# Optimization experiments

Hardware: AMD Instinct MI355X
Metric: run time of the kernel (lower is better)

Reference implementation:

```python
import jax, jax.numpy as jnp
import numpy as np
import math

D_MODEL, D_K, D_V, H = 512, 64, 64, 8

def setup_inputs() -> dict:
    key = jax.random.key(0)
    ks = jax.random.split(key, 8)
    B, L = 2, 4096
    q = jax.random.normal(ks[0], (B, L, D_MODEL), dtype=jnp.float32)
    k = jax.random.normal(ks[1], (B, L, D_MODEL), dtype=jnp.float32)
    v = jax.random.normal(ks[2], (B, L, D_MODEL), dtype=jnp.float32)
    attention_mask = jnp.ones((B, L), dtype=jnp.int32)
    s = 1.0 / math.sqrt(D_MODEL)
    Wq = jax.random.uniform(ks[3], (D_MODEL, H * D_K), dtype=jnp.float32, minval=-s, maxval=s)
    Wk = jax.random.uniform(ks[4], (D_MODEL, H * D_K), dtype=jnp.float32, minval=-s, maxval=s)
    Wv = jax.random.uniform(ks[5], (D_MODEL, H * D_V), dtype=jnp.float32, minval=-s, maxval=s)
    so = 1.0 / math.sqrt(H * D_V)
    Wo = jax.random.uniform(ks[6], (H * D_V, D_MODEL), dtype=jnp.float32, minval=-so, maxval=so)
    return {"q": q, "k": k, "v": v, "attention_mask": attention_mask,
            "Wq": Wq, "Wk": Wk, "Wv": Wv, "Wo": Wo}

def reference(q, k, v, attention_mask, Wq, Wk, Wv, Wo):
    B, L, _ = q.shape
    scale = 1.0 / math.sqrt(D_K)
    # project and split heads: [B, H, L, d]
    qh = (q @ Wq).reshape(B, L, H, D_K).transpose(0, 2, 1, 3)
    kh = (k @ Wk).reshape(B, L, H, D_K).transpose(0, 2, 1, 3)
    vh = (v @ Wv).reshape(B, L, H, D_V).transpose(0, 2, 1, 3)
    score = jnp.einsum('bhqd,bhkd->bhqk', qh, kh) * scale  # [B,H,L,L]
    mask = attention_mask[:, None, None, :]  # [B,1,1,L]
    score = jnp.where(mask == 0, -jnp.inf, score)
    attn = jax.nn.softmax(score, axis=-1)
    out = jnp.einsum('bhqk,bhkd->bhqd', attn, vh)
    out = out.transpose(0, 2, 1, 3).reshape(B, L, H * D_V)
    return out @ Wo
```

## Files before the change

### kernel.cpp

```cpp
#include <hip/hip_runtime.h>

typedef short bf16x8 __attribute__((ext_vector_type(8)));
typedef float f32x4 __attribute__((ext_vector_type(4)));
typedef unsigned short u16x8 __attribute__((ext_vector_type(8)));

static __device__ __forceinline__ unsigned short f2bf(float f) {
  unsigned int x = __builtin_bit_cast(unsigned int, f);
  x += 0x7FFFu + ((x >> 16) & 1u);
  return (unsigned short)(x >> 16);
}
static __device__ __forceinline__ unsigned int pk2bf(float a, float b) {
  unsigned int ia = __builtin_bit_cast(unsigned int, a) + 0x8000u;
  unsigned int ib = __builtin_bit_cast(unsigned int, b) + 0x8000u;
  return __builtin_amdgcn_perm(ib, ia, 0x07060302u);
}
static __device__ __forceinline__ void gl2lds16(const unsigned short* g, unsigned short* l) {
  __builtin_amdgcn_global_load_lds(
      (const __attribute__((address_space(1))) unsigned int*)g,
      (__attribute__((address_space(3))) unsigned int*)l, 16, 0, 0);
}

__global__ __launch_bounds__(256) void cvt3(const float* __restrict__ q, const float* __restrict__ k,
                                            const float* __restrict__ v,
                                            unsigned short* __restrict__ qo, unsigned short* __restrict__ ko,
                                            unsigned short* __restrict__ vo) {
  const float* src = (blockIdx.y == 0) ? q : (blockIdx.y == 1) ? k : v;
  unsigned short* dst = (blockIdx.y == 0) ? qo : (blockIdx.y == 1) ? ko : vo;
  int i = (blockIdx.x * 256 + threadIdx.x) * 8;
  float4 a = *(const float4*)(src + i);
  float4 b = *(const float4*)(src + i + 4);
  uint4 pk;
  pk.x = pk2bf(a.x, a.y); pk.y = pk2bf(a.z, a.w);
  pk.z = pk2bf(b.x, b.y); pk.w = pk2bf(b.z, b.w);
  *(uint4*)(dst + i) = pk;
}

__global__ __launch_bounds__(256) void wtrans4(const float* __restrict__ Wq, const float* __restrict__ Wk,
                                               const float* __restrict__ Wv, const float* __restrict__ Wo,
                                               unsigned short* __restrict__ WT) {
  __shared__ __align__(16) float T[64 * 68];
  const int z = blockIdx.z;
  const float* W = (z == 0) ? Wq : (z == 1) ? Wk : (z == 2) ? Wv : Wo;
  unsigned short* out = WT + (size_t)z * 512 * 512;
  const int k0 = blockIdx.x * 64, n0 = blockIdx.y * 64;
  const int tid = threadIdx.x;
#pragma unroll
  for (int i = 0; i < 4; ++i) {
    int chunk = i * 256 + tid;
    int row = chunk >> 4, fc = chunk & 15;
    *(float4*)(T + row * 68 + fc * 4) =
        *(const float4*)(W + (size_t)(k0 + row) * 512 + n0 + fc * 4);
  }
  __syncthreads();
#pragma unroll
  for (int i = 0; i < 2; ++i) {
    int chunk = i * 256 + tid;
    int nr = chunk >> 3, kc = chunk & 7;
    u16x8 v;
#pragma unroll
    for (int j = 0; j < 8; ++j) v[j] = f2bf(T[(kc * 8 + j) * 68 + nr]);
    *(u16x8*)(out + (size_t)(n0 + nr) * 512 + k0 + kc * 8) = v;
  }
}

__global__ __launch_bounds__(256) void gemm_qkv(const unsigned short* __restrict__ Aq,
                                                const unsigned short* __restrict__ Ak,
                                                const unsigned short* __restrict__ Av,
                                                const unsigned short* __restrict__ Bt,
                                                unsigned short* __restrict__ C,
                                                float qscale) {
  __shared__ __align__(16) unsigned short Abuf[2][128 * 64];
  __shared__ __align__(16) unsigned short Bbuf[2][64 * 64];
  const int K = 512, LDC = 1536;
  const unsigned short* A = (blockIdx.y < 8) ? Aq : (blockIdx.y < 16) ? Ak : Av;
  const float scale = (blockIdx.y < 8) ? qscale : 1.0f;
  const int tid = threadIdx.x;
  const int wid = tid >> 6, lane = tid & 63, quad = lane >> 4, li = lane & 15;
  const int bm = blockIdx.x * 128, bn = blockIdx.y * 64;
  const int wm = wid * 32;
  const unsigned short* ga[4]; int oa[4];
  const unsigned short* gb[2]; int ob[2];
#pragma unroll
  for (int i = 0; i < 4; ++i) {
    int lam = i * 256 + wid * 64 + lane;
    int r = lam >> 3, c = (lam & 7) ^ (r & 7);
    ga[i] = A + (size_t)(bm + r) * K + c * 8;
    oa[i] = lam * 8;
  }
#pragma unroll
  for (int i = 0; i < 2; ++i) {
    int lam = i * 256 + wid * 64 + lane;
    int r = lam >> 3, c = (lam & 7) ^ (r & 7);
    gb[i] = Bt + (size_t)(bn + r) * K + c * 8;
    ob[i] = lam * 8;
  }
#pragma unroll
  for (int i = 0; i < 4; ++i) { gl2lds16(ga[i], &Abuf[0][oa[i]]); ga[i] += 64; }
#pragma unroll
  for (int i = 0; i < 2; ++i) { gl2lds16(gb[i], &Bbuf[0][ob[i]]); gb[i] += 64; }

  f32x4 acc[2][4] = {};
  const int sw = li & 7;
  for (int s = 0; s < 8; ++s) {
    __builtin_amdgcn_s_barrier();
    if (s + 1 < 8) {
      int p = (s + 1) & 1;
#pragma unroll
      for (int i = 0; i < 4; ++i) { gl2lds16(ga[i], &Abuf[p][oa[i]]); ga[i] += 64; }
#pragma unroll
      for (int i = 0; i < 2; ++i) { gl2lds16(gb[i], &Bbuf[p][ob[i]]); gb[i] += 64; }
      asm volatile("s_waitcnt vmcnt(6)" ::: "memory");
    } else {
      asm volatile("s_waitcnt vmcnt(0)" ::: "memory");
    }
    __builtin_amdgcn_s_barrier();
    __builtin_amdgcn_sched_barrier(0);
    const unsigned short* As = &Abuf[s & 1][0];
    const unsigned short* Bs = &Bbuf[s & 1][0];
#pragma unroll
    for (int kk = 0; kk < 2; ++kk) {
      bf16x8 af[2], bfr[4];
#pragma unroll
      for (int t = 0; t < 2; ++t)
        af[t] = *(const bf16x8*)(As + (wm + t * 16 + li) * 64 + (((kk * 4 + quad) ^ sw) * 8));
#pragma unroll
      for (int t = 0; t < 4; ++t)
        bfr[t] = *(const bf16x8*)(Bs + (t * 16 + li) * 64 + (((kk * 4 + quad) ^ sw) * 8));
#pragma unroll
      for (int mt = 0; mt < 2; ++mt)
#pragma unroll
        for (int nt = 0; nt < 4; ++nt)
          acc[mt][nt] = __builtin_amdgcn_mfma_f32_16x16x32_bf16(af[mt], bfr[nt], acc[mt][nt], 0, 0, 0);
    }
  }
#pragma unroll
  for (int mt = 0; mt < 2; ++mt)
#pragma unroll
    for (int nt = 0; nt < 4; ++nt) {
      int r0 = bm + wm + mt * 16 + quad * 4;
      int c  = bn + nt * 16 + li;
#pragma unroll
      for (int r = 0; r < 4; ++r)
        C[(size_t)(r0 + r) * LDC + c] = f2bf(acc[mt][nt][r] * scale);
    }
}

__global__ __launch_bounds__(256) void gemm_o(const unsigned short* __restrict__ A,
                                              const unsigned short* __restrict__ Bt,
                                              float* __restrict__ Cf) {
  __shared__ __align__(16) unsigned short Abuf[2][128 * 64];
  __shared__ __align__(16) unsigned short Bbuf[2][64 * 64];
  const int K = 512, LDC = 512;
  const int tid = threadIdx.x;
  const int wid = tid >> 6, lane = tid & 63, quad = lane >> 4, li = lane & 15;
  const int bm = blockIdx.x * 128, bn = blockIdx.y * 64;
  const int wm = wid * 32;
  const unsigned short* ga[4]; int oa[4];
  const unsigned short* gb[2]; int ob[2];
#pragma unroll
  for (int i = 0; i < 4; ++i) {
    int lam = i * 256 + wid * 64 + lane;
    int r = lam >> 3, c = (lam & 7) ^ (r & 7);
    ga[i] = A + (size_t)(bm + r) * K + c * 8;
    oa[i] = lam * 8;
  }
#pragma unroll
  for (int i = 0; i < 2; ++i) {
    int lam = i * 256 + wid * 64 + lane;
    int r = lam >> 3, c = (lam & 7) ^ (r & 7);
    gb[i] = Bt + (size_t)(bn + r) * K + c * 8;
    ob[i] = lam * 8;
  }
#pragma unroll
  for (int i = 0; i < 4; ++i) { gl2lds16(ga[i], &Abuf[0][oa[i]]); ga[i] += 64; }
#pragma unroll
  for (int i = 0; i < 2; ++i) { gl2lds16(gb[i], &Bbuf[0][ob[i]]); gb[i] += 64; }

  f32x4 acc[2][4] = {};
  const int sw = li & 7;
  for (int s = 0; s < 8; ++s) {
    __builtin_amdgcn_s_barrier();
    if (s + 1 < 8) {
      int p = (s + 1) & 1;
#pragma unroll
      for (int i = 0; i < 4; ++i) { gl2lds16(ga[i], &Abuf[p][oa[i]]); ga[i] += 64; }
#pragma unroll
      for (int i = 0; i < 2; ++i) { gl2lds16(gb[i], &Bbuf[p][ob[i]]); gb[i] += 64; }
      asm volatile("s_waitcnt vmcnt(6)" ::: "memory");
    } else {
      asm volatile("s_waitcnt vmcnt(0)" ::: "memory");
    }
    __builtin_amdgcn_s_barrier();
    __builtin_amdgcn_sched_barrier(0);
    const unsigned short* As = &Abuf[s & 1][0];
    const unsigned short* Bs = &Bbuf[s & 1][0];
#pragma unroll
    for (int kk = 0; kk < 2; ++kk) {
      bf16x8 af[2], bfr[4];
#pragma unroll
      for (int t = 0; t < 2; ++t)
        af[t] = *(const bf16x8*)(As + (wm + t * 16 + li) * 64 + (((kk * 4 + quad) ^ sw) * 8));
#pragma unroll
      for (int t = 0; t < 4; ++t)
        bfr[t] = *(const bf16x8*)(Bs + (t * 16 + li) * 64 + (((kk * 4 + quad) ^ sw) * 8));
#pragma unroll
      for (int mt = 0; mt < 2; ++mt)
#pragma unroll
        for (int nt = 0; nt < 4; ++nt)
          acc[mt][nt] = __builtin_amdgcn_mfma_f32_16x16x32_bf16(af[mt], bfr[nt], acc[mt][nt], 0, 0, 0);
    }
  }
#pragma unroll
  for (int mt = 0; mt < 2; ++mt)
#pragma unroll
    for (int nt = 0; nt < 4; ++nt) {
      int r0 = bm + wm + mt * 16 + quad * 4;
      int c  = bn + nt * 16 + li;
#pragma unroll
      for (int r = 0; r < 4; ++r)
        Cf[(size_t)(r0 + r) * LDC + c] = acc[mt][nt][r];
    }
}

__global__ __launch_bounds__(256) void vtrans(const unsigned short* __restrict__ qkv,
                                              unsigned short* __restrict__ vt) {
  __shared__ __align__(16) unsigned short T[64 * 72];
  const int kt = blockIdx.x;
  const int bh = blockIdx.y;
  const int b = bh >> 3, h = bh & 7;
  const int tid = threadIdx.x;
#pragma unroll
  for (int i = 0; i < 2; ++i) {
    int chunk = i * 256 + tid;
    int row = chunk >> 3, c8 = chunk & 7;
    *(uint4*)(T + row * 72 + c8 * 8) =
        *(const uint4*)(qkv + (size_t)(b * 4096 + kt * 64 + row) * 1536 + 1024 + h * 64 + c8 * 8);
  }
  __syncthreads();
#pragma unroll
  for (int i = 0; i < 2; ++i) {
    int chunk = i * 256 + tid;
    int dr = chunk >> 3, c8 = chunk & 7;
    u16x8 v;
#pragma unroll
    for (int j = 0; j < 8; ++j) v[j] = T[(c8 * 8 + j) * 72 + dr];
    *(u16x8*)(vt + (size_t)(bh * 64 + dr) * 4096 + kt * 64 + c8 * 8) = v;
  }
}

__global__ __launch_bounds__(512) void attn(const unsigned short* __restrict__ qkv,
                                            const unsigned short* __restrict__ vt,
                                            const int* __restrict__ mask,
                                            unsigned short* __restrict__ obuf) {
  __shared__ __align__(16) unsigned short Kbuf[2][64 * 64];
  __shared__ __align__(16) unsigned short Vbuf[2][64 * 64];
  __shared__ __align__(16) unsigned short Psh[8][16 * 72];
  __shared__ __align__(16) unsigned short MskBits[256];
  const int qt = blockIdx.x, h = blockIdx.y, b = blockIdx.z;
  const int tid = threadIdx.x;
  const int wid = tid >> 6, lane = tid & 63, quad = lane >> 4, li = lane & 15;
  const size_t tok0 = (size_t)b * 4096;

  if (tid < 256) {
    const int4* mp = (const int4*)(mask + b * 4096 + tid * 16);
    unsigned int bits = 0;
#pragma unroll
    for (int j = 0; j < 4; ++j) {
      int4 m4 = mp[j];
      bits |= (m4.x ? 1u : 0u) << (j * 4 + 0);
      bits |= (m4.y ? 1u : 0u) << (j * 4 + 1);
      bits |= (m4.z ? 1u : 0u) << (j * 4 + 2);
      bits |= (m4.w ? 1u : 0u) << (j * 4 + 3);
    }
    MskBits[tid] = (unsigned short)bits;
  }

  const unsigned short* qp = qkv + (tok0 + qt * 128 + wid * 16 + li) * 1536 + h * 64;
  bf16x8 bq0 = *(const bf16x8*)(qp + quad * 8);
  bf16x8 bq1 = *(const bf16x8*)(qp + 32 + quad * 8);

  const unsigned short* kbase = qkv + tok0 * 1536 + 512 + h * 64;
  const unsigned short* vbase = vt + (size_t)(b * 8 + h) * 64 * 4096;
  const int wk = wid & 3;
  const int lam0 = wk * 128 + lane, lam1 = lam0 + 64;
  const int r0 = lam0 >> 3, c0 = (lam0 & 7) ^ (r0 & 7);
  const int r1 = lam1 >> 3, c1 = (lam1 & 7) ^ (r1 & 7);
  const unsigned short *g0, *g1;
  size_t kstride;
  unsigned short *lb0, *lb1;
  if (wid < 4) {
    g0 = kbase + (size_t)r0 * 1536 + c0 * 8;
    g1 = kbase + (size_t)r1 * 1536 + c1 * 8;
    kstride = (size_t)64 * 1536;
    lb0 = &Kbuf[0][0]; lb1 = &Kbuf[1][0];
  } else {
    g0 = vbase + (size_t)r0 * 4096 + c0 * 8;
    g1 = vbase + (size_t)r1 * 4096 + c1 * 8;
    kstride = 64;
    lb0 = &Vbuf[0][0]; lb1 = &Vbuf[1][0];
  }
  const int o0 = lam0 * 8, o1 = lam1 * 8;

  gl2lds16(g0, lb0 + o0);
  gl2lds16(g1, lb0 + o1);
  g0 += kstride; g1 += kstride;

  f32x4 lacc = {};
  f32x4 accO[4] = {};
  unsigned short* Pw = &Psh[wid][0];
  const int sw = li & 7;

  asm volatile("s_waitcnt lgkmcnt(0)" ::: "memory");

  for (int t = 0; t < 64; ++t) {
    __builtin_amdgcn_s_barrier();
    if (t < 63) {
      unsigned short* lb = ((t + 1) & 1) ? lb1 : lb0;
      gl2lds16(g0, lb + o0);
      gl2lds16(g1, lb + o1);
      g0 += kstride; g1 += kstride;
      asm volatile("s_waitcnt vmcnt(2)" ::: "memory");
    } else {
      asm volatile("s_waitcnt vmcnt(0)" ::: "memory");
    }
    __builtin_amdgcn_s_barrier();
    __builtin_amdgcn_sched_barrier(0);
    const unsigned short* Ks = &Kbuf[t & 1][0];
    const unsigned short* Vs = &Vbuf[t & 1][0];

    f32x4 s[4];
    __builtin_amdgcn_s_setprio(1);
#pragma unroll
    for (int kb = 0; kb < 4; ++kb) {
      const unsigned short* kr = Ks + (kb * 16 + li) * 64;
      bf16x8 ak0 = *(const bf16x8*)(kr + ((quad ^ sw) * 8));
      bf16x8 ak1 = *(const bf16x8*)(kr + (((4 + quad) ^ sw) * 8));
      f32x4 z = {};
      z = __builtin_amdgcn_mfma_f32_16x16x32_bf16(ak0, bq0, z, 0, 0, 0);
      z = __builtin_amdgcn_mfma_f32_16x16x32_bf16(ak1, bq1, z, 0, 0, 0);
      s[kb] = z;
    }
    __builtin_amdgcn_s_setprio(0);
    unsigned long long mbits = *(const unsigned long long*)(MskBits + t * 4);
    if (mbits != ~0ull) {
#pragma unroll
      for (int kb = 0; kb < 4; ++kb)
#pragma unroll
        for (int r = 0; r < 4; ++r) {
          int key = kb * 16 + quad * 4 + r;
          if (!((mbits >> key) & 1ull)) s[kb][r] = -1e30f;
        }
    }
#pragma unroll
    for (int kb = 0; kb < 4; ++kb) {
#pragma unroll
      for (int r = 0; r < 4; ++r) s[kb][r] = __builtin_amdgcn_exp2f(s[kb][r]);
      lacc += s[kb];
      uint2 pk;
      pk.x = pk2bf(s[kb][0], s[kb][1]);
      pk.y = pk2bf(s[kb][2], s[kb][3]);
      *(uint2*)(Pw + li * 72 + kb * 16 + quad * 4) = pk;
    }
    bf16x8 p0 = *(const bf16x8*)(Pw + li * 72 + quad * 8);
    bf16x8 p1 = *(const bf16x8*)(Pw + li * 72 + 32 + quad * 8);
    __builtin_amdgcn_s_setprio(1);
#pragma unroll
    for (int dc = 0; dc < 4; ++dc) {
      const unsigned short* vr = Vs + (dc * 16 + li) * 64;
      bf16x8 bv0 = *(const bf16x8*)(vr + ((quad ^ sw) * 8));
      bf16x8 bv1 = *(const bf16x8*)(vr + (((4 + quad) ^ sw) * 8));
      accO[dc] = __builtin_amdgcn_mfma_f32_16x16x32_bf16(p0, bv0, accO[dc], 0, 0, 0);
      accO[dc] = __builtin_amdgcn_mfma_f32_16x16x32_bf16(p1, bv1, accO[dc], 0, 0, 0);
    }
    __builtin_amdgcn_s_setprio(0);
  }
  float lt = lacc[0] + lacc[1] + lacc[2] + lacc[3];
  lt += __shfl_xor(lt, 16);
  lt += __shfl_xor(lt, 32);
  float lv0 = 1.f / __shfl(lt, quad * 4 + 0);
  float lv1 = 1.f / __shfl(lt, quad * 4 + 1);
  float lv2 = 1.f / __shfl(lt, quad * 4 + 2);
  float lv3 = 1.f / __shfl(lt, quad * 4 + 3);
#pragma unroll
  for (int dc = 0; dc < 4; ++dc) {
    size_t r0q = tok0 + qt * 128 + wid * 16 + quad * 4;
    size_t col = h * 64 + dc * 16 + li;
    obuf[(r0q + 0) * 512 + col] = f2bf(accO[dc][0] * lv0);
    obuf[(r0q + 1) * 512 + col] = f2bf(accO[dc][1] * lv1);
    obuf[(r0q + 2) * 512 + col] = f2bf(accO[dc][2] * lv2);
    obuf[(r0q + 3) * 512 + col] = f2bf(accO[dc][3] * lv3);
  }
}

extern "C" void kernel_launch(void* const* d_in, const int* in_sizes, int n_in,
                              void* d_out, int out_size, void* d_ws, size_t ws_size,
                              hipStream_t stream) {
  const float* q  = (const float*)d_in[0];
  const float* k  = (const float*)d_in[1];
  const float* v  = (const float*)d_in[2];
  const int* mask = (const int*)d_in[3];
  const float* Wq = (const float*)d_in[4];
  const float* Wk = (const float*)d_in[5];
  const float* Wv = (const float*)d_in[6];
  const float* Wo = (const float*)d_in[7];
  float* out = (float*)d_out;

  char* ws = (char*)d_ws;
  const size_t SA = (size_t)8192 * 512 * 2;
  unsigned short* qbf  = (unsigned short*)(ws);
  unsigned short* kbf  = (unsigned short*)(ws + SA);
  unsigned short* vbf  = (unsigned short*)(ws + 2 * SA);
  unsigned short* qkvh = (unsigned short*)(ws + 3 * SA);
  unsigned short* wAll = (unsigned short*)(ws + 6 * SA);
  unsigned short* woT  = wAll + (size_t)3 * 512 * 512;
  unsigned short* vtb  = qbf;
  unsigned short* ob   = kbf;

  dim3 cg(2048, 3);
  cvt3<<<cg, 256, 0, stream>>>(q, k, v, qbf, kbf, vbf);
  dim3 wg(8, 8, 4);
  wtrans4<<<wg, 256, 0, stream>>>(Wq, Wk, Wv, Wo, wAll);
  const float qscale = 0.125f * 1.44269504f;
  dim3 gq(64, 24);
  gemm_qkv<<<gq, 256, 0, stream>>>(qbf, kbf, vbf, wAll, qkvh, qscale);
  dim3 vg(64, 16);
  vtrans<<<vg, 256, 0, stream>>>(qkvh, vtb);
  dim3 ag(32, 8, 2);
  attn<<<ag, 512, 0, stream>>>(qkvh, vtb, mask, ob);
  dim3 go(64, 8);
  gemm_o<<<go, 256, 0, stream>>>(ob, woT, out);
}
```

Baseline: 222.8 us.

## Give each attention wave two query tiles and drop LDS round-trip for P

The attention block shrinks from 8 to 4 waves, with each wave now handling 32 query rows as two 16-row groups, so every K and V fragment read from LDS feeds twice as many MFMAs. The V-transpose kernel permutes key order so the S accumulator layout can be packed straight into the bf16 P operand in registers, removing the per-wave P shared-memory buffer and its store/load. This cuts LDS traffic and instructions per tile, at the cost of more registers per wave and fewer waves to hide latency.

```diff
diff --git a/kernel.cpp b/kernel.cpp
--- a/kernel.cpp
+++ b/kernel.cpp
@@ -243,25 +243,29 @@
     int dr = chunk >> 3, c8 = chunk & 7;
     u16x8 v;
 #pragma unroll
-    for (int j = 0; j < 8; ++j) v[j] = T[(c8 * 8 + j) * 72 + dr];
+    for (int j = 0; j < 8; ++j) {
+      int p = c8 * 8 + j;
+      int ph = p & 31;
+      int lk = (p & 32) | (((ph >> 2) & 1) << 4) | (((ph >> 3) & 3) << 2) | (ph & 3);
+      v[j] = T[lk * 72 + dr];
+    }
     *(u16x8*)(vt + (size_t)(bh * 64 + dr) * 4096 + kt * 64 + c8 * 8) = v;
   }
 }
 
-__global__ __launch_bounds__(512) void attn(const unsigned short* __restrict__ qkv,
+__global__ __launch_bounds__(256) void attn(const unsigned short* __restrict__ qkv,
                                             const unsigned short* __restrict__ vt,
                                             const int* __restrict__ mask,
                                             unsigned short* __restrict__ obuf) {
   __shared__ __align__(16) unsigned short Kbuf[2][64 * 64];
   __shared__ __align__(16) unsigned short Vbuf[2][64 * 64];
-  __shared__ __align__(16) unsigned short Psh[8][16 * 72];
   __shared__ __align__(16) unsigned short MskBits[256];
   const int qt = blockIdx.x, h = blockIdx.y, b = blockIdx.z;
   const int tid = threadIdx.x;
   const int wid = tid >> 6, lane = tid & 63, quad = lane >> 4, li = lane & 15;
   const size_t tok0 = (size_t)b * 4096;
 
-  if (tid < 256) {
+  {
     const int4* mp = (const int4*)(mask + b * 4096 + tid * 16);
     unsigned int bits = 0;
 #pragma unroll
@@ -275,39 +279,30 @@
     MskBits[tid] = (unsigned short)bits;
   }
 
-  const unsigned short* qp = qkv + (tok0 + qt * 128 + wid * 16 + li) * 1536 + h * 64;
-  bf16x8 bq0 = *(const bf16x8*)(qp + quad * 8);
-  bf16x8 bq1 = *(const bf16x8*)(qp + 32 + quad * 8);
+  const unsigned short* qp0 = qkv + (tok0 + qt * 128 + wid * 32 + li) * 1536 + h * 64;
+  const unsigned short* qp1 = qp0 + (size_t)16 * 1536;
+  bf16x8 bq[2][2];
+  bq[0][0] = *(const bf16x8*)(qp0 + quad * 8);
+  bq[0][1] = *(const bf16x8*)(qp0 + 32 + quad * 8);
+  bq[1][0] = *(const bf16x8*)(qp1 + quad * 8);
+  bq[1][1] = *(const bf16x8*)(qp1 + 32 + quad * 8);
 
   const unsigned short* kbase = qkv + tok0 * 1536 + 512 + h * 64;
   const unsigned short* vbase = vt + (size_t)(b * 8 + h) * 64 * 4096;
-  const int wk = wid & 3;
-  const int lam0 = wk * 128 + lane, lam1 = lam0 + 64;
-  const int r0 = lam0 >> 3, c0 = (lam0 & 7) ^ (r0 & 7);
-  const int r1 = lam1 >> 3, c1 = (lam1 & 7) ^ (r1 & 7);
-  const unsigned short *g0, *g1;
-  size_t kstride;
-  unsigned short *lb0, *lb1;
-  if (wid < 4) {
-    g0 = kbase + (size_t)r0 * 1536 + c0 * 8;
-    g1 = kbase + (size_t)r1 * 1536 + c1 * 8;
-    kstride = (size_t)64 * 1536;
-    lb0 = &Kbuf[0][0]; lb1 = &Kbuf[1][0];
-  } else {
-    g0 = vbase + (size_t)r0 * 4096 + c0 * 8;
-    g1 = vbase + (size_t)r1 * 4096 + c1 * 8;
-    kstride = 64;
-    lb0 = &Vbuf[0][0]; lb1 = &Vbuf[1][0];
-  }
-  const int o0 = lam0 * 8, o1 = lam1 * 8;
-
-  gl2lds16(g0, lb0 + o0);
-  gl2lds16(g1, lb0 + o1);
-  g0 += kstride; g1 += kstride;
-
-  f32x4 lacc = {};
-  f32x4 accO[4] = {};
-  unsigned short* Pw = &Psh[wid][0];
+  const int l0 = tid,       sr0 = l0 >> 3, sc0 = (l0 & 7) ^ (sr0 & 7);
+  const int l1 = 256 + tid, sr1 = l1 >> 3, sc1 = (l1 & 7) ^ (sr1 & 7);
+  const unsigned short* gk0 = kbase + (size_t)sr0 * 1536 + sc0 * 8;
+  const unsigned short* gk1 = kbase + (size_t)sr1 * 1536 + sc1 * 8;
+  const unsigned short* gv0 = vbase + (size_t)sr0 * 4096 + sc0 * 8;
+  const unsigned short* gv1 = vbase + (size_t)sr1 * 4096 + sc1 * 8;
+  const int ok0 = l0 * 8, ok1 = l1 * 8;
+
+  gl2lds16(gk0, &Kbuf[0][ok0]); gl2lds16(gk1, &Kbuf[0][ok1]);
+  gl2lds16(gv0, &Vbuf[0][ok0]); gl2lds16(gv1, &Vbuf[0][ok1]);
+  gk0 += (size_t)64 * 1536; gk1 += (size_t)64 * 1536; gv0 += 64; gv1 += 64;
+
+  f32x4 lacc[2] = {};
+  f32x4 accO[2][4] = {};
   const int sw = li & 7;
 
   asm volatile("s_waitcnt lgkmcnt(0)" ::: "memory");
@@ -315,11 +310,11 @@
   for (int t = 0; t < 64; ++t) {
     __builtin_amdgcn_s_barrier();
     if (t < 63) {
-      unsigned short* lb = ((t + 1) & 1) ? lb1 : lb0;
-      gl2lds16(g0, lb + o0);
-      gl2lds16(g1, lb + o1);
-      g0 += kstride; g1 += kstride;
-      asm volatile("s_waitcnt vmcnt(2)" ::: "memory");
+      int p = (t + 1) & 1;
+      gl2lds16(gk0, &Kbuf[p][ok0]); gl2lds16(gk1, &Kbuf[p][ok1]);
+      gl2lds16(gv0, &Vbuf[p][ok0]); gl2lds16(gv1, &Vbuf[p][ok1]);
+      gk0 += (size_t)64 * 1536; gk1 += (size_t)64 * 1536; gv0 += 64; gv1 += 64;
+      asm volatile("s_waitcnt vmcnt(4)" ::: "memory");
     } else {
       asm volatile("s_waitcnt vmcnt(0)" ::: "memory");
     }
@@ -328,17 +323,20 @@
     const unsigned short* Ks = &Kbuf[t & 1][0];
     const unsigned short* Vs = &Vbuf[t & 1][0];
 
-    f32x4 s[4];
+    f32x4 s[2][4];
     __builtin_amdgcn_s_setprio(1);
 #pragma unroll
     for (int kb = 0; kb < 4; ++kb) {
       const unsigned short* kr = Ks + (kb * 16 + li) * 64;
       bf16x8 ak0 = *(const bf16x8*)(kr + ((quad ^ sw) * 8));
       bf16x8 ak1 = *(const bf16x8*)(kr + (((4 + quad) ^ sw) * 8));
-      f32x4 z = {};
-      z = __builtin_amdgcn_mfma_f32_16x16x32_bf16(ak0, bq0, z, 0, 0, 0);
-      z = __builtin_amdgcn_mfma_f32_16x16x32_bf16(ak1, bq1, z, 0, 0, 0);
-      s[kb] = z;
+#pragma unroll
+      for (int qg = 0; qg < 2; ++qg) {
+        f32x4 z = {};
+        z = __builtin_amdgcn_mfma_f32_16x16x32_bf16(ak0, bq[qg][0], z, 0, 0, 0);
+        z = __builtin_amdgcn_mfma_f32_16x16x32_bf16(ak1, bq[qg][1], z, 0, 0, 0);
+        s[qg][kb] = z;
+      }
     }
     __builtin_amdgcn_s_setprio(0);
     unsigned long long mbits = *(const unsigned long long*)(MskBits + t * 4);
@@ -348,47 +346,58 @@
 #pragma unroll
         for (int r = 0; r < 4; ++r) {
           int key = kb * 16 + quad * 4 + r;
-          if (!((mbits >> key) & 1ull)) s[kb][r] = -1e30f;
+          if (!((mbits >> key) & 1ull)) { s[0][kb][r] = -1e30f; s[1][kb][r] = -1e30f; }
         }
     }
-#pragma unroll
-    for (int kb = 0; kb < 4; ++kb) {
-#pragma unroll
-      for (int r = 0; r < 4; ++r) s[kb][r] = __builtin_amdgcn_exp2f(s[kb][r]);
-      lacc += s[kb];
-      uint2 pk;
-      pk.x = pk2bf(s[kb][0], s[kb][1]);
-      pk.y = pk2bf(s[kb][2], s[kb][3]);
-      *(uint2*)(Pw + li * 72 + kb * 16 + quad * 4) = pk;
-    }
-    bf16x8 p0 = *(const bf16x8*)(Pw + li * 72 + quad * 8);
-    bf16x8 p1 = *(const bf16x8*)(Pw + li * 72 + 32 + quad * 8);
+    bf16x8 pf[2][2];
+#pragma unroll
+    for (int qg = 0; qg < 2; ++qg) {
+#pragma unroll
+      for (int kb = 0; kb < 4; ++kb) {
+#pragma unroll
+        for (int r = 0; r < 4; ++r) s[qg][kb][r] = __builtin_amdgcn_exp2f(s[qg][kb][r]);
+        lacc[qg] += s[qg][kb];
+      }
+      uint4 u0, u1;
+      u0.x = pk2bf(s[qg][0][0], s[qg][0][1]); u0.y = pk2bf(s[qg][0][2], s[qg][0][3]);
+      u0.z = pk2bf(s[qg][1][0], s[qg][1][1]); u0.w = pk2bf(s[qg][1][2], s[qg][1][3]);
+      u1.x = pk2bf(s[qg][2][0], s[qg][2][1]); u1.y = pk2bf(s[qg][2][2], s[qg][2][3]);
+      u1.z = pk2bf(s[qg][3][0], s[qg][3][1]); u1.w = pk2bf(s[qg][3][2], s[qg][3][3]);
+      pf[qg][0] = __builtin_bit_cast(bf16x8, u0);
+      pf[qg][1] = __builtin_bit_cast(bf16x8, u1);
+    }
     __builtin_amdgcn_s_setprio(1);
 #pragma unroll
     for (int dc = 0; dc < 4; ++dc) {
       const unsigned short* vr = Vs + (dc * 16 + li) * 64;
       bf16x8 bv0 = *(const bf16x8*)(vr + ((quad ^ sw) * 8));
       bf16x8 bv1 = *(const bf16x8*)(vr + (((4 + quad) ^ sw) * 8));
-      accO[dc] = __builtin_amdgcn_mfma_f32_16x16x32_bf16(p0, bv0, accO[dc], 0, 0, 0);
-      accO[dc] = __builtin_amdgcn_mfma_f32_16x16x32_bf16(p1, bv1, accO[dc], 0, 0, 0);
+#pragma unroll
+      for (int qg = 0; qg < 2; ++qg) {
+        accO[qg][dc] = __builtin_amdgcn_mfma_f32_16x16x32_bf16(pf[qg][0], bv0, accO[qg][dc], 0, 0, 0);
+        accO[qg][dc] = __builtin_amdgcn_mfma_f32_16x16x32_bf16(pf[qg][1], bv1, accO[qg][dc], 0, 0, 0);
+      }
     }
     __builtin_amdgcn_s_setprio(0);
   }
-  float lt = lacc[0] + lacc[1] + lacc[2] + lacc[3];
-  lt += __shfl_xor(lt, 16);
-  lt += __shfl_xor(lt, 32);
-  float lv0 = 1.f / __shfl(lt, quad * 4 + 0);
-  float lv1 = 1.f / __shfl(lt, quad * 4 + 1);
-  float lv2 = 1.f / __shfl(lt, quad * 4 + 2);
-  float lv3 = 1.f / __shfl(lt, quad * 4 + 3);
-#pragma unroll
-  for (int dc = 0; dc < 4; ++dc) {
-    size_t r0q = tok0 + qt * 128 + wid * 16 + quad * 4;
-    size_t col = h * 64 + dc * 16 + li;
-    obuf[(r0q + 0) * 512 + col] = f2bf(accO[dc][0] * lv0);
-    obuf[(r0q + 1) * 512 + col] = f2bf(accO[dc][1] * lv1);
-    obuf[(r0q + 2) * 512 + col] = f2bf(accO[dc][2] * lv2);
-    obuf[(r0q + 3) * 512 + col] = f2bf(accO[dc][3] * lv3);
+#pragma unroll
+  for (int qg = 0; qg < 2; ++qg) {
+    float lt = lacc[qg][0] + lacc[qg][1] + lacc[qg][2] + lacc[qg][3];
+    lt += __shfl_xor(lt, 16);
+    lt += __shfl_xor(lt, 32);
+    float lv0 = 1.f / __shfl(lt, quad * 4 + 0);
+    float lv1 = 1.f / __shfl(lt, quad * 4 + 1);
+    float lv2 = 1.f / __shfl(lt, quad * 4 + 2);
+    float lv3 = 1.f / __shfl(lt, quad * 4 + 3);
+    size_t r0q = tok0 + qt * 128 + wid * 32 + qg * 16 + quad * 4;
+#pragma unroll
+    for (int dc = 0; dc < 4; ++dc) {
+      size_t col = h * 64 + dc * 16 + li;
+      obuf[(r0q + 0) * 512 + col] = f2bf(accO[qg][dc][0] * lv0);
+      obuf[(r0q + 1) * 512 + col] = f2bf(accO[qg][dc][1] * lv1);
+      obuf[(r0q + 2) * 512 + col] = f2bf(accO[qg][dc][2] * lv2);
+      obuf[(r0q + 3) * 512 + col] = f2bf(accO[qg][dc][3] * lv3);
+    }
   }
 }
 
@@ -426,7 +435,7 @@
   dim3 vg(64, 16);
   vtrans<<<vg, 256, 0, stream>>>(qkvh, vtb);
   dim3 ag(32, 8, 2);
-  attn<<<ag, 512, 0, stream>>>(qkvh, vtb, mask, ob);
+  attn<<<ag, 256, 0, stream>>>(qkvh, vtb, mask, ob);
   dim3 go(64, 8);
   gemm_o<<<go, 256, 0, stream>>>(ob, woT, out);
 }
```

After: 243.2 us. 9.2% more time.
